# Kernel tuning notes

Measured on AMD Instinct MI355X. Metric: run time of the kernel, lower is better.

## Reference

```python
import jax, jax.numpy as jnp
import numpy as np

N = 32768
D_IN = 1728   # 192*3*3
D = 1024
C_CLS = 2


def setup_inputs() -> dict:
    key = jax.random.key(0)
    ks = jax.random.split(key, 8)
    # _initialize_weights: Linear weights ~ N(0, 0.01), biases zero
    x = jax.random.normal(ks[0], (N, D_IN), dtype=jnp.float32)
    w1 = jax.random.normal(ks[1], (D, D_IN), dtype=jnp.float32) * 0.01
    b1 = jnp.zeros((D,), jnp.float32)
    w2 = jax.random.normal(ks[2], (D, D), dtype=jnp.float32) * 0.01
    b2 = jnp.zeros((D,), jnp.float32)
    w_fc = jax.random.normal(ks[3], (C_CLS, D), dtype=jnp.float32) * 0.01
    b_fc = jnp.zeros((C_CLS,), jnp.float32)
    w_q = jax.random.normal(ks[4], (D, D), dtype=jnp.float32) * 0.01
    b_q = jnp.zeros((D,), jnp.float32)
    w_v = jax.random.normal(ks[5], (D, D), dtype=jnp.float32) * 0.01
    b_v = jnp.zeros((D,), jnp.float32)
    # Conv1d(2,2,kernel_size=1024): weight [out=2, in=2, k=1024]
    fan = C_CLS * D
    w_fcc = jax.random.uniform(ks[6], (C_CLS, C_CLS, D), jnp.float32,
                               -1.0 / np.sqrt(fan), 1.0 / np.sqrt(fan))
    b_fcc = jax.random.uniform(ks[7], (C_CLS,), jnp.float32,
                               -1.0 / np.sqrt(fan), 1.0 / np.sqrt(fan))
    return {"x": x, "w1": w1, "b1": b1, "w2": w2, "b2": b2,
            "w_fc": w_fc, "b_fc": b_fc, "w_q": w_q, "b_q": b_q,
            "w_v": w_v, "b_v": b_v, "w_fcc": w_fcc, "b_fcc": b_fcc}


def reference(x, w1, b1, w2, b2, w_fc, b_fc, w_q, b_q, w_v, b_v, w_fcc, b_fcc):
    # classifier MLP (dropout = identity in eval)
    h = jax.nn.relu(x @ w1.T + b1)          # [N, 1024]
    feat = jax.nn.relu(h @ w2.T + b2)       # [N, 1024]
    instance_pred = feat @ w_fc.T + b_fc    # [N, 2]
    V = feat @ w_v.T + b_v                  # [N, 1024]
    Q = feat @ w_q.T + b_q                  # [N, 1024]
    # torch.sort(..., descending=True)[1][0] == argmax per class column
    top_idx = jnp.argmax(instance_pred, axis=0)   # [2]
    m_feats = feat[top_idx]                 # [2, 1024]
    q_max = m_feats @ w_q.T + b_q           # [2, 1024]
    scale = jnp.sqrt(jnp.float32(Q.shape[1]))
    A = jax.nn.softmax((Q @ q_max.T) / scale, axis=0)  # softmax over instances, [N, 2]
    B = A.T @ V                             # [2, 1024]
    # Conv1d(2,2,k=1024) over length-1024 input -> single output position
    C = (jnp.einsum('oik,ik->o', w_fcc, B) + b_fcc).reshape(1, C_CLS)
    return instance_pred, C, A, B[None]
```

## Files before the change

kernel.cpp:

```cpp
#include <hip/hip_runtime.h>
#include <stdint.h>


typedef unsigned short u16;
typedef __attribute__((ext_vector_type(8))) short short8;
typedef __attribute__((ext_vector_type(4))) float floatx4;

#define TILE 128
#define BK 32

__device__ __forceinline__ float bf2f(u16 u) {
  union { unsigned u; float f; } x; x.u = ((unsigned)u) << 16; return x.f;
}
__device__ __forceinline__ u16 f2bf(float f) {
  union { float f; unsigned u; } x; x.f = f;
  return (u16)((x.u + 0x7fffu + ((x.u >> 16) & 1u)) >> 16);
}
__device__ __forceinline__ unsigned ordf(float f) {
  union { float f; unsigned u; } x; x.f = f;
  return (x.u & 0x80000000u) ? ~x.u : (x.u | 0x80000000u);
}
__device__ __forceinline__ void gload16(const void* g, void* l) {
  __builtin_amdgcn_global_load_lds(
      (const __attribute__((address_space(1))) void*)g,
      (__attribute__((address_space(3))) void*)l, 16, 0, 0);
}

template <int MODE>
__global__ __launch_bounds__(256) void gemm_bt(
    const u16* __restrict__ A, const u16* __restrict__ B,
    const float* __restrict__ bias, u16* __restrict__ O,
    float* __restrict__ OL, int K, int ntiles, int ldo) {
  __shared__ __align__(16) u16 As[TILE * BK];
  __shared__ __align__(16) u16 Bs[TILE * BK];

  const int xcd = blockIdx.x & 7;
  const int j = blockIdx.x >> 3;
  const int mstride = gridDim.x / (ntiles << 3);
  const int mt = xcd * mstride + j / ntiles;
  const int nt = j % ntiles;
  const int m0 = mt * TILE, n0 = nt * TILE;
  const int tid = threadIdx.x;
  const int lane = tid & 63;
  const int wm = (tid >> 7) * 64;
  const int wn = ((tid >> 6) & 1) * 64;

  floatx4 acc[4][4];
#pragma unroll
  for (int i = 0; i < 4; ++i)
#pragma unroll
    for (int jf = 0; jf < 4; ++jf) acc[i][jf] = (floatx4){0.f, 0.f, 0.f, 0.f};

  const int srow = tid >> 2;
  const int sq = ((tid & 3) - srow) & 3;
  const u16* Ag0 = A + (size_t)(m0 + srow) * K + sq * 8;
  const u16* Ag1 = Ag0 + (size_t)64 * K;
  const u16* Bg0 = B + (size_t)(n0 + srow) * K + sq * 8;
  const u16* Bg1 = Bg0 + (size_t)64 * K;
  u16* Al0 = As + tid * 8;
  u16* Al1 = Al0 + 256 * 8;
  u16* Bl0 = Bs + tid * 8;
  u16* Bl1 = Bl0 + 256 * 8;

  const int fr = lane & 15;
  const int fq = lane >> 4;
  const u16* Af = As + (size_t)(wm + fr) * BK + (((fq + fr) & 3) * 8);
  const u16* Bf = Bs + (size_t)(wn + fr) * BK + (((fq + fr) & 3) * 8);

  const int kiters = K / BK;
  for (int kt = 0; kt < kiters; ++kt) {
    gload16(Ag0, Al0); gload16(Ag1, Al1);
    gload16(Bg0, Bl0); gload16(Bg1, Bl1);
    Ag0 += BK; Ag1 += BK; Bg0 += BK; Bg1 += BK;
    __syncthreads();
    short8 a[4], b[4];
#pragma unroll
    for (int f = 0; f < 4; ++f) {
      a[f] = *(const short8*)(Af + f * 16 * BK);
      b[f] = *(const short8*)(Bf + f * 16 * BK);
    }
#pragma unroll
    for (int i = 0; i < 4; ++i)
#pragma unroll
      for (int jf = 0; jf < 4; ++jf)
        acc[i][jf] = __builtin_amdgcn_mfma_f32_16x16x32_bf16(a[i], b[jf],
                                                             acc[i][jf], 0, 0, 0);
    __syncthreads();
  }

  const int er = (lane >> 4) * 4;
  const int ec = lane & 15;
  if (MODE == 0 || n0 < 1024) {
#pragma unroll
    for (int jf = 0; jf < 4; ++jf) {
      const int col = n0 + wn + jf * 16 + ec;
      const float bv = bias[col];
#pragma unroll
      for (int i = 0; i < 4; ++i) {
        const int row = m0 + wm + i * 16 + er;
#pragma unroll
        for (int r = 0; r < 4; ++r) {
          float v = acc[i][jf][r] + bv;
          if (MODE == 0) v = fmaxf(v, 0.f);
          O[(size_t)(row + r) * ldo + col] = f2bf(v);
        }
      }
    }
  } else {
    if (wn == 0 && ec < 2) {
#pragma unroll
      for (int i = 0; i < 4; ++i) {
        const int row = m0 + wm + i * 16 + er;
#pragma unroll
        for (int r = 0; r < 4; ++r)
          OL[(size_t)(row + r) * 2 + ec] = acc[i][0][r];
      }
    }
  }
}

__global__ void k_init(u16* b3pad, float* Bbuf, unsigned long long* keys) {
  int i = blockIdx.x * 256 + threadIdx.x;
  if (i < 129024) b3pad[i] = 0;
  if (i < 2048) Bbuf[i] = 0.f;
  if (i < 2) keys[i] = 0ull;
}

__global__ void k_cast(const float* __restrict__ s, u16* __restrict__ d, int n4) {
  int i = blockIdx.x * 256 + threadIdx.x;
  if (i >= n4) return;
  float4 v = ((const float4*)s)[i];
  unsigned long long o = (unsigned long long)f2bf(v.x) |
                         ((unsigned long long)f2bf(v.y) << 16) |
                         ((unsigned long long)f2bf(v.z) << 32) |
                         ((unsigned long long)f2bf(v.w) << 48);
  ((unsigned long long*)d)[i] = o;
}

__global__ __launch_bounds__(256) void k_ip(const u16* __restrict__ feat,
                                            const float* __restrict__ wfc,
                                            const float* __restrict__ bfc,
                                            float* __restrict__ out_ip) {
  const int row = blockIdx.x * 4 + (threadIdx.x >> 6);
  const int lane = threadIdx.x & 63;
  const u16* fr = feat + (size_t)row * 1024 + lane * 16;
  const float* w0 = wfc + lane * 16;
  const float* w1 = wfc + 1024 + lane * 16;
  float s0 = 0.f, s1 = 0.f;
#pragma unroll
  for (int t = 0; t < 16; ++t) {
    float f = bf2f(fr[t]);
    s0 += f * w0[t];
    s1 += f * w1[t];
  }
#pragma unroll
  for (int off = 32; off > 0; off >>= 1) {
    s0 += __shfl_down(s0, off, 64);
    s1 += __shfl_down(s1, off, 64);
  }
  if (lane == 0) {
    out_ip[(size_t)row * 2 + 0] = s0 + bfc[0];
    out_ip[(size_t)row * 2 + 1] = s1 + bfc[1];
  }
}

__global__ __launch_bounds__(256) void k_argmax(const float* __restrict__ ip,
                                                unsigned long long* __restrict__ keys) {
  float m0 = -1e30f, m1 = -1e30f;
  int i0 = 0, i1 = 0;
  for (int i = blockIdx.x * 256 + threadIdx.x; i < 32768; i += 256 * 64) {
    float v0 = ip[2 * i], v1 = ip[2 * i + 1];
    if (v0 > m0) { m0 = v0; i0 = i; }
    if (v1 > m1) { m1 = v1; i1 = i; }
  }
  unsigned long long k0 =
      ((unsigned long long)ordf(m0) << 32) | (0xFFFFFFFFu - (unsigned)i0);
  unsigned long long k1 =
      ((unsigned long long)ordf(m1) << 32) | (0xFFFFFFFFu - (unsigned)i1);
#pragma unroll
  for (int off = 32; off > 0; off >>= 1) {
    unsigned long long t0 = __shfl_down(k0, off, 64);
    unsigned long long t1 = __shfl_down(k1, off, 64);
    if (t0 > k0) k0 = t0;
    if (t1 > k1) k1 = t1;
  }
  __shared__ unsigned long long s0[4], s1[4];
  const int lane = threadIdx.x & 63, wv = threadIdx.x >> 6;
  if (lane == 0) { s0[wv] = k0; s1[wv] = k1; }
  __syncthreads();
  if (threadIdx.x == 0) {
    for (int w = 1; w < 4; ++w) {
      if (s0[w] > k0) k0 = s0[w];
      if (s1[w] > k1) k1 = s1[w];
    }
    atomicMax(keys + 0, k0);
    atomicMax(keys + 1, k1);
  }
}

__global__ __launch_bounds__(256) void k_qmax(const u16* __restrict__ feat,
                                              const float* __restrict__ wq,
                                              const float* __restrict__ bq,
                                              const unsigned long long* __restrict__ keys,
                                              float* __restrict__ qmax) {
  const int gw = blockIdx.x * 4 + (threadIdx.x >> 6);
  const int c = gw >> 10, k = gw & 1023;
  const int lane = threadIdx.x & 63;
  const int idx = (int)(0xFFFFFFFFu - (unsigned)(keys[c] & 0xFFFFFFFFull));
  const u16* fr = feat + (size_t)idx * 1024 + lane * 16;
  const float* wr = wq + (size_t)k * 1024 + lane * 16;
  float s = 0.f;
#pragma unroll
  for (int t = 0; t < 16; ++t) s += bf2f(fr[t]) * wr[t];
#pragma unroll
  for (int off = 32; off > 0; off >>= 1) s += __shfl_down(s, off, 64);
  if (lane == 0) qmax[c * 1024 + k] = s + bq[k];
}

__global__ __launch_bounds__(256) void k_t(const float* __restrict__ wq,
                                           const float* __restrict__ qmax,
                                           float* __restrict__ tpart) {
  const int jb = blockIdx.x & 3, kp = blockIdx.x >> 2;
  const int jcol = jb * 256 + threadIdx.x;
  float s0 = 0.f, s1 = 0.f;
  for (int k = kp * 128; k < kp * 128 + 128; ++k) {
    float w = wq[(size_t)k * 1024 + jcol];
    s0 += qmax[k] * w;
    s1 += qmax[1024 + k] * w;
  }
  tpart[kp * 2048 + jcol] = s0;
  tpart[kp * 2048 + 1024 + jcol] = s1;
}

__global__ __launch_bounds__(256) void k_tcast(const float* __restrict__ tpart,
                                               u16* __restrict__ b3) {
  const int i = blockIdx.x * 256 + threadIdx.x;
  float s = 0.f;
#pragma unroll
  for (int kp = 0; kp < 8; ++kp) s += tpart[kp * 2048 + i];
  b3[(size_t)(1024 + (i >> 10)) * 1024 + (i & 1023)] = f2bf(s);
}

__global__ __launch_bounds__(256) void k_reduce(const float* __restrict__ lg,
                                                float* __restrict__ ms) {
  __shared__ float r0[256], r1[256];
  const int tid = threadIdx.x;
  float m0 = -1e30f, m1 = -1e30f;
  for (int i = tid; i < 32768; i += 256) {
    m0 = fmaxf(m0, lg[2 * i]);
    m1 = fmaxf(m1, lg[2 * i + 1]);
  }
  r0[tid] = m0; r1[tid] = m1;
  __syncthreads();
  for (int s = 128; s > 0; s >>= 1) {
    if (tid < s) {
      r0[tid] = fmaxf(r0[tid], r0[tid + s]);
      r1[tid] = fmaxf(r1[tid], r1[tid + s]);
    }
    __syncthreads();
  }
  m0 = r0[0]; m1 = r1[0];
  __syncthreads();
  float s0 = 0.f, s1 = 0.f;
  for (int i = tid; i < 32768; i += 256) {
    s0 += __expf((lg[2 * i] - m0) * 0.03125f);
    s1 += __expf((lg[2 * i + 1] - m1) * 0.03125f);
  }
  r0[tid] = s0; r1[tid] = s1;
  __syncthreads();
  for (int s = 128; s > 0; s >>= 1) {
    if (tid < s) { r0[tid] += r0[tid + s]; r1[tid] += r1[tid + s]; }
    __syncthreads();
  }
  if (tid == 0) { ms[0] = m0; ms[1] = m1; ms[2] = r0[0]; ms[3] = r1[0]; }
}

__global__ __launch_bounds__(256) void k_ab(const float* __restrict__ lg,
                                            const float* __restrict__ ms,
                                            const u16* __restrict__ V,
                                            float* __restrict__ outA,
                                            float* __restrict__ Bbuf) {
  const int tid = threadIdx.x;
  const int row0 = blockIdx.x * 128;
  const float m0 = ms[0], m1 = ms[1];
  const float inv0 = 1.f / ms[2], inv1 = 1.f / ms[3];
  {
    const int r = row0 + (tid >> 1);
    const int c = tid & 1;
    outA[2 * r + c] =
        __expf((lg[2 * r + c] - (c ? m1 : m0)) * 0.03125f) * (c ? inv1 : inv0);
  }
  float p0[4] = {0, 0, 0, 0}, p1[4] = {0, 0, 0, 0};
  const int kb = tid * 4;
  for (int r = row0; r < row0 + 128; ++r) {
    const float a0 = __expf((lg[2 * r] - m0) * 0.03125f) * inv0;
    const float a1 = __expf((lg[2 * r + 1] - m1) * 0.03125f) * inv1;
    unsigned long long vv = *(const unsigned long long*)(V + (size_t)r * 1024 + kb);
    float f0 = bf2f((u16)vv), f1 = bf2f((u16)(vv >> 16));
    float f2 = bf2f((u16)(vv >> 32)), f3 = bf2f((u16)(vv >> 48));
    p0[0] += a0 * f0; p0[1] += a0 * f1; p0[2] += a0 * f2; p0[3] += a0 * f3;
    p1[0] += a1 * f0; p1[1] += a1 * f1; p1[2] += a1 * f2; p1[3] += a1 * f3;
  }
#pragma unroll
  for (int t = 0; t < 4; ++t) {
    atomicAdd(&Bbuf[kb + t], p0[t]);
    atomicAdd(&Bbuf[1024 + kb + t], p1[t]);
  }
}

__global__ __launch_bounds__(256) void k_c(const float* __restrict__ Bbuf,
                                           const float* __restrict__ wfcc,
                                           const float* __restrict__ bfcc,
                                           float* __restrict__ outC,
                                           float* __restrict__ outB) {
  __shared__ float r0[256], r1[256];
  const int tid = threadIdx.x;
  float s0 = 0.f, s1 = 0.f;
  for (int i = tid; i < 2048; i += 256) {
    float b = Bbuf[i];
    outB[i] = b;
    s0 += wfcc[i] * b;
    s1 += wfcc[2048 + i] * b;
  }
  r0[tid] = s0; r1[tid] = s1;
  __syncthreads();
  for (int s = 128; s > 0; s >>= 1) {
    if (tid < s) { r0[tid] += r0[tid + s]; r1[tid] += r1[tid + s]; }
    __syncthreads();
  }
  if (tid == 0) {
    outC[0] = r0[0] + bfcc[0];
    outC[1] = r1[0] + bfcc[1];
  }
}

extern "C" void kernel_launch(void* const* d_in, const int* in_sizes, int n_in,
                              void* d_out, int out_size, void* d_ws, size_t ws_size,
                              hipStream_t stream) {
  const float* x    = (const float*)d_in[0];
  const float* w1   = (const float*)d_in[1];
  const float* b1   = (const float*)d_in[2];
  const float* w2   = (const float*)d_in[3];
  const float* b2   = (const float*)d_in[4];
  const float* wfc  = (const float*)d_in[5];
  const float* bfc  = (const float*)d_in[6];
  const float* wq   = (const float*)d_in[7];
  const float* bq   = (const float*)d_in[8];
  const float* wv   = (const float*)d_in[9];
  const float* bv   = (const float*)d_in[10];
  const float* wfcc = (const float*)d_in[11];
  const float* bfcc = (const float*)d_in[12];

  float* out   = (float*)d_out;
  float* outIP = out;
  float* outC  = out + 65536;
  float* outA  = out + 65538;
  float* outB  = out + 131074;

  char* ws = (char*)d_ws;
  u16* XB  = (u16*)(ws);
  u16* HB  = (u16*)(ws + 113246208);
  u16* FB  = (u16*)(ws + 180355072);
  u16* W1B = (u16*)(ws + 247463936);
  float* TPART = (float*)(ws + 247463936);
  u16* W2B = (u16*)(ws + 251002880);
  u16* B3  = (u16*)(ws + 253100032);
  float* LG = (float*)(ws + 255459328);
  float* QM = (float*)(ws + 255721472);
  unsigned long long* KEYS = (unsigned long long*)(ws + 255729664);
  float* MS   = (float*)(ws + 255729680);
  float* BBUF = (float*)(ws + 255729696);

  k_init<<<504, 256, 0, stream>>>(B3 + 1026 * 1024, BBUF, KEYS);
  k_cast<<<55296, 256, 0, stream>>>(x, XB, 56623104 / 4);
  k_cast<<<1728, 256, 0, stream>>>(w1, W1B, 1769472 / 4);
  k_cast<<<1024, 256, 0, stream>>>(w2, W2B, 1048576 / 4);
  k_cast<<<1024, 256, 0, stream>>>(wv, B3, 1048576 / 4);

  gemm_bt<0><<<256 * 8, 256, 0, stream>>>(XB, W1B, b1, HB, nullptr, 1728, 8, 1024);
  gemm_bt<0><<<256 * 8, 256, 0, stream>>>(HB, W2B, b2, FB, nullptr, 1024, 8, 1024);

  k_ip<<<8192, 256, 0, stream>>>(FB, wfc, bfc, outIP);
  k_argmax<<<64, 256, 0, stream>>>(outIP, KEYS);
  k_qmax<<<512, 256, 0, stream>>>(FB, wq, bq, KEYS, QM);
  k_t<<<32, 256, 0, stream>>>(wq, QM, TPART);
  k_tcast<<<8, 256, 0, stream>>>(TPART, B3);

  gemm_bt<1><<<256 * 9, 256, 0, stream>>>(FB, B3, bv, HB, LG, 1024, 9, 1024);

  k_reduce<<<1, 256, 0, stream>>>(LG, MS);
  k_ab<<<256, 256, 0, stream>>>(LG, MS, HB, outA, BBUF);
  k_c<<<1, 256, 0, stream>>>(BBUF, wfcc, bfcc, outC, outB);
}
```

Baseline: 854.3 us.

## Double-buffer GEMM LDS tiles, stage epilogue through LDS, fuse prep kernels

The GEMM main loop now uses two LDS buffers. The next k-tile's global-to-LDS loads are issued while the current tile feeds the MFMAs, and this removes one barrier per iteration. The epilogue writes bf16 results to LDS first and then stores coalesced 16-byte rows to global memory, replacing scattered 2-byte stores. The init kernel and four cast launches are merged into one k_prep kernel to cut launch overhead, at the cost of doubled LDS use per block and possibly lower occupancy.

New measurement: 923.7 us. +8.1%, slower.

```diff
diff --git a/kernel.cpp b/kernel.cpp
--- a/kernel.cpp
+++ b/kernel.cpp
@@ -31,8 +31,7 @@
     const u16* __restrict__ A, const u16* __restrict__ B,
     const float* __restrict__ bias, u16* __restrict__ O,
     float* __restrict__ OL, int K, int ntiles, int ldo) {
-  __shared__ __align__(16) u16 As[TILE * BK];
-  __shared__ __align__(16) u16 Bs[TILE * BK];
+  __shared__ __align__(16) u16 SH[16384];
 
   const int xcd = blockIdx.x & 7;
   const int j = blockIdx.x >> 3;
@@ -57,27 +56,38 @@
   const u16* Ag1 = Ag0 + (size_t)64 * K;
   const u16* Bg0 = B + (size_t)(n0 + srow) * K + sq * 8;
   const u16* Bg1 = Bg0 + (size_t)64 * K;
-  u16* Al0 = As + tid * 8;
-  u16* Al1 = Al0 + 256 * 8;
-  u16* Bl0 = Bs + tid * 8;
-  u16* Bl1 = Bl0 + 256 * 8;
+  u16* const ASl[2] = {SH + tid * 8, SH + 4096 + tid * 8};
+  u16* const BSl[2] = {SH + 8192 + tid * 8, SH + 12288 + tid * 8};
 
   const int fr = lane & 15;
   const int fq = lane >> 4;
-  const u16* Af = As + (size_t)(wm + fr) * BK + (((fq + fr) & 3) * 8);
-  const u16* Bf = Bs + (size_t)(wn + fr) * BK + (((fq + fr) & 3) * 8);
+  const int fo = (size_t)0;
+  const u16* const AF[2] = {
+      SH + (wm + fr) * BK + (((fq + fr) & 3) * 8),
+      SH + 4096 + (wm + fr) * BK + (((fq + fr) & 3) * 8)};
+  const u16* const BF[2] = {
+      SH + 8192 + (wn + fr) * BK + (((fq + fr) & 3) * 8),
+      SH + 12288 + (wn + fr) * BK + (((fq + fr) & 3) * 8)};
+  (void)fo;
+
+  gload16(Ag0, ASl[0]); gload16(Ag1, ASl[0] + 2048);
+  gload16(Bg0, BSl[0]); gload16(Bg1, BSl[0] + 2048);
+  Ag0 += BK; Ag1 += BK; Bg0 += BK; Bg1 += BK;
 
   const int kiters = K / BK;
   for (int kt = 0; kt < kiters; ++kt) {
-    gload16(Ag0, Al0); gload16(Ag1, Al1);
-    gload16(Bg0, Bl0); gload16(Bg1, Bl1);
-    Ag0 += BK; Ag1 += BK; Bg0 += BK; Bg1 += BK;
+    const int cur = kt & 1, nxt = cur ^ 1;
     __syncthreads();
+    if (kt + 1 < kiters) {
+      gload16(Ag0, ASl[nxt]); gload16(Ag1, ASl[nxt] + 2048);
+      gload16(Bg0, BSl[nxt]); gload16(Bg1, BSl[nxt] + 2048);
+      Ag0 += BK; Ag1 += BK; Bg0 += BK; Bg1 += BK;
+    }
     short8 a[4], b[4];
 #pragma unroll
     for (int f = 0; f < 4; ++f) {
-      a[f] = *(const short8*)(Af + f * 16 * BK);
-      b[f] = *(const short8*)(Bf + f * 16 * BK);
+      a[f] = *(const short8*)(AF[cur] + f * 16 * BK);
+      b[f] = *(const short8*)(BF[cur] + f * 16 * BK);
     }
 #pragma unroll
     for (int i = 0; i < 4; ++i)
@@ -85,28 +95,11 @@
       for (int jf = 0; jf < 4; ++jf)
         acc[i][jf] = __builtin_amdgcn_mfma_f32_16x16x32_bf16(a[i], b[jf],
                                                              acc[i][jf], 0, 0, 0);
-    __syncthreads();
-  }
-
-  const int er = (lane >> 4) * 4;
-  const int ec = lane & 15;
-  if (MODE == 0 || n0 < 1024) {
-#pragma unroll
-    for (int jf = 0; jf < 4; ++jf) {
-      const int col = n0 + wn + jf * 16 + ec;
-      const float bv = bias[col];
-#pragma unroll
-      for (int i = 0; i < 4; ++i) {
-        const int row = m0 + wm + i * 16 + er;
-#pragma unroll
-        for (int r = 0; r < 4; ++r) {
-          float v = acc[i][jf][r] + bv;
-          if (MODE == 0) v = fmaxf(v, 0.f);
-          O[(size_t)(row + r) * ldo + col] = f2bf(v);
-        }
-      }
-    }
-  } else {
+  }
+
+  const int er = fq * 4;
+  const int ec = fr;
+  if (MODE == 1 && n0 >= 1024) {
     if (wn == 0 && ec < 2) {
 #pragma unroll
       for (int i = 0; i < 4; ++i) {
@@ -116,19 +109,56 @@
           OL[(size_t)(row + r) * 2 + ec] = acc[i][0][r];
       }
     }
-  }
-}
-
-__global__ void k_init(u16* b3pad, float* Bbuf, unsigned long long* keys) {
-  int i = blockIdx.x * 256 + threadIdx.x;
-  if (i < 129024) b3pad[i] = 0;
-  if (i < 2048) Bbuf[i] = 0.f;
-  if (i < 2) keys[i] = 0ull;
-}
-
-__global__ void k_cast(const float* __restrict__ s, u16* __restrict__ d, int n4) {
-  int i = blockIdx.x * 256 + threadIdx.x;
-  if (i >= n4) return;
+    return;
+  }
+
+  __syncthreads();
+#pragma unroll
+  for (int jf = 0; jf < 4; ++jf) {
+    const int col = wn + jf * 16 + ec;
+    const float bv = bias[n0 + col];
+#pragma unroll
+    for (int i = 0; i < 4; ++i) {
+      const int row = wm + i * 16 + er;
+#pragma unroll
+      for (int r = 0; r < 4; ++r) {
+        float v = acc[i][jf][r] + bv;
+        if (MODE == 0) v = fmaxf(v, 0.f);
+        SH[(row + r) * TILE + col] = f2bf(v);
+      }
+    }
+  }
+  __syncthreads();
+#pragma unroll
+  for (int c = 0; c < 8; ++c) {
+    const int flat = c * 256 + tid;
+    const int row = flat >> 4, ch = flat & 15;
+    short8 v = *(const short8*)(SH + flat * 8);
+    *(short8*)(O + (size_t)(m0 + row) * ldo + n0 + ch * 8) = v;
+  }
+}
+
+__global__ void k_prep(const float* __restrict__ x, const float* __restrict__ w1,
+                       const float* __restrict__ w2, const float* __restrict__ wv,
+                       u16* __restrict__ XB, u16* __restrict__ W1B,
+                       u16* __restrict__ W2B, u16* __restrict__ B3,
+                       float* __restrict__ Bbuf, unsigned long long* __restrict__ keys) {
+  int b = blockIdx.x;
+  const int tid = threadIdx.x;
+  const float* s; u16* d;
+  if (b < 55296) { s = x; d = XB; }
+  else if ((b -= 55296) < 1728) { s = w1; d = W1B; }
+  else if ((b -= 1728) < 1024) { s = w2; d = W2B; }
+  else if ((b -= 1024) < 1024) { s = wv; d = B3; }
+  else {
+    b -= 1024;
+    int i = b * 256 + tid;
+    if (i < 129024) B3[1026 * 1024 + i] = 0;
+    if (i < 2048) Bbuf[i] = 0.f;
+    if (i < 2) keys[i] = 0ull;
+    return;
+  }
+  int i = b * 256 + tid;
   float4 v = ((const float4*)s)[i];
   unsigned long long o = (unsigned long long)f2bf(v.x) |
                          ((unsigned long long)f2bf(v.y) << 16) |
@@ -371,11 +401,8 @@
   float* MS   = (float*)(ws + 255729680);
   float* BBUF = (float*)(ws + 255729696);
 
-  k_init<<<504, 256, 0, stream>>>(B3 + 1026 * 1024, BBUF, KEYS);
-  k_cast<<<55296, 256, 0, stream>>>(x, XB, 56623104 / 4);
-  k_cast<<<1728, 256, 0, stream>>>(w1, W1B, 1769472 / 4);
-  k_cast<<<1024, 256, 0, stream>>>(w2, W2B, 1048576 / 4);
-  k_cast<<<1024, 256, 0, stream>>>(wv, B3, 1048576 / 4);
+  k_prep<<<55296 + 1728 + 1024 + 1024 + 505, 256, 0, stream>>>(
+      x, w1, w2, wv, XB, W1B, W2B, B3, BBUF, KEYS);
 
   gemm_bt<0><<<256 * 8, 256, 0, stream>>>(XB, W1B, b1, HB, nullptr, 1728, 8, 1024);
   gemm_bt<0><<<256 * 8, 256, 0, stream>>>(HB, W2B, b2, FB, nullptr, 1024, 8, 1024);
```
